# Performance work log

Measured on AMD Instinct MI355X. Metric: run time of the kernel, lower is better.

## Reference

```python
import jax, jax.numpy as jnp
import numpy as np

L = 12            # label_size (10 real tags + START + END)
START_ID = 10
END_ID = 11
V, E, T, B, HD = 32000, 512, 512, 64, 1024
H = HD // 2       # per-direction hidden size


def setup_inputs() -> dict:
    key = jax.random.key(0)
    ks = jax.random.split(key, 12)
    inp = {}
    inp['sents'] = jax.random.randint(ks[0], (B, T), 0, V)
    inp['labels'] = jax.random.randint(ks[1], (B, T), 0, L - 2)
    inp['lengths'] = jax.random.randint(ks[2], (B,), T // 2, T + 1)
    inp['embedding'] = jax.random.normal(ks[3], (V, E), jnp.float32) * 0.1
    s_ih = float(np.sqrt(6.0 / (4 * H + E)))
    s_hh = float(np.sqrt(6.0 / (4 * H + H)))
    # PyTorch LSTM gate order: i, f, g, o ; forget-gate bias init to 1 in each of
    # b_ih and b_hh -> combined bias has 2.0 in the forget slice.
    b = jnp.zeros((4 * H,), jnp.float32).at[H:2 * H].set(2.0)
    inp['w_ih_f'] = jax.random.uniform(ks[4], (4 * H, E), jnp.float32, -s_ih, s_ih)
    inp['w_hh_f'] = jax.random.uniform(ks[5], (4 * H, H), jnp.float32, -s_hh, s_hh)
    inp['b_f'] = b
    inp['w_ih_r'] = jax.random.uniform(ks[6], (4 * H, E), jnp.float32, -s_ih, s_ih)
    inp['w_hh_r'] = jax.random.uniform(ks[7], (4 * H, H), jnp.float32, -s_hh, s_hh)
    inp['b_r'] = b
    s_fc = float(np.sqrt(6.0 / (L + HD)))
    inp['fc_w'] = jax.random.uniform(ks[8], (L, HD), jnp.float32, -s_fc, s_fc)
    inp['fc_b'] = jnp.zeros((L,), jnp.float32)
    trans = jax.random.normal(ks[9], (L, L), jnp.float32)
    trans = trans.at[:, START_ID].set(-1000.0).at[END_ID, :].set(-1000.0)
    inp['transitions'] = trans
    return inp


def _lstm_dir(x, w_ih, w_hh, b, reverse):
    # x: [B, T, E] -> hidden states [B, T, H]; zero initial state.
    xg = jnp.einsum('bte,ge->btg', x, w_ih) + b  # [B, T, 4H] precomputed input gates
    if reverse:
        xg = xg[:, ::-1]
    h0 = jnp.zeros((x.shape[0], H), x.dtype)

    def step(carry, g):
        h, c = carry
        g = g + h @ w_hh.T
        i, f, gg, o = jnp.split(g, 4, axis=-1)
        c = jax.nn.sigmoid(f) * c + jax.nn.sigmoid(i) * jnp.tanh(gg)
        h = jax.nn.sigmoid(o) * jnp.tanh(c)
        return (h, c), h

    _, hs = jax.lax.scan(step, (h0, h0), jnp.swapaxes(xg, 0, 1))
    hs = jnp.swapaxes(hs, 0, 1)  # [B, T, H]
    if reverse:
        hs = hs[:, ::-1]
    return hs


def _features(sents, embedding, w_ih_f, w_hh_f, b_f, w_ih_r, w_hh_r, b_r, fc_w, fc_b):
    embeds = embedding[sents]  # [B, T, E]
    fwd = _lstm_dir(embeds, w_ih_f, w_hh_f, b_f, reverse=False)
    rev = _lstm_dir(embeds, w_ih_r, w_hh_r, b_r, reverse=True)
    out = jnp.tanh(jnp.concatenate([fwd, rev], axis=-1))  # [B, T, 2H]
    return jnp.einsum('bth,lh->btl', out, fc_w) + fc_b    # [B, T, L]


def _crf_log_z(feats, trans, lengths):
    # Batched forward algorithm; faithful to the original (alpha0 = zeros).
    def step(alpha, xs):
        feat_t, t = xs
        new = jax.nn.logsumexp(alpha[:, :, None] + trans[None] + feat_t[:, None, :], axis=1)
        return jnp.where((t < lengths)[:, None], new, alpha), None

    alpha0 = jnp.zeros((feats.shape[0], L), feats.dtype)
    alpha, _ = jax.lax.scan(step, alpha0, (jnp.swapaxes(feats, 0, 1), jnp.arange(feats.shape[1])))
    return jax.nn.logsumexp(alpha + trans[None, :, END_ID], axis=1)  # [B]


def _gold_scores(feats, trans, labels, lengths):
    Bv, Tv, _ = feats.shape
    lab_ext = jnp.concatenate([jnp.full((Bv, 1), START_ID, labels.dtype), labels], axis=1)
    prev, nxt = lab_ext[:, :-1], lab_ext[:, 1:]  # [B, T]
    emit = jnp.take_along_axis(feats, nxt[:, :, None], axis=2)[..., 0]
    tr = trans[prev, nxt]
    mask = (jnp.arange(Tv)[None, :] < lengths[:, None]).astype(feats.dtype)
    score = jnp.sum((emit + tr) * mask, axis=1)
    last = jnp.take_along_axis(labels, (lengths - 1)[:, None], axis=1)[:, 0]
    return score + trans[last, END_ID]  # [B]


def reference(sents, labels, lengths, embedding, w_ih_f, w_hh_f, b_f,
              w_ih_r, w_hh_r, b_r, fc_w, fc_b, transitions):
    feats = _features(sents, embedding, w_ih_f, w_hh_f, b_f, w_ih_r, w_hh_r, b_r, fc_w, fc_b)
    log_z = _crf_log_z(feats, transitions, lengths)
    gold = _gold_scores(feats, transitions, labels, lengths)
    return jnp.sum(log_z - gold)  # neg_log_likelihood summed over batch
```

## Files before the change

### kernel.cpp

```cpp
#include <hip/hip_runtime.h>
#include <stdint.h>

#define Bz 64
#define Tz 512
#define Ez 512
#define Hz 512
#define Lz 12
#define START_ID 10
#define END_ID 11

typedef unsigned int uint32;
typedef unsigned long long uint64;
typedef unsigned short ushort16;
typedef __bf16 bf16x8 __attribute__((ext_vector_type(8)));
typedef float f32x4 __attribute__((ext_vector_type(4)));

__device__ __forceinline__ float bf2f(uint32 u) {
    return __uint_as_float(u << 16);
}
__device__ __forceinline__ ushort16 f2bf(float f) {
    uint32 x = __float_as_uint(f);
    x += 0x7FFFu + ((x >> 16) & 1u);
    return (ushort16)(x >> 16);
}
__device__ __forceinline__ float sigf(float x) {
    return 1.0f / (1.0f + __expf(-x));
}
__device__ __forceinline__ float tanh_fast(float x) {
    return 1.0f - 2.0f / (__expf(2.0f * x) + 1.0f);
}
__device__ __forceinline__ bf16x8 packbf8(float4 a, float4 b) {
    union { ushort16 u[8]; bf16x8 v; } r;
    r.u[0] = f2bf(a.x); r.u[1] = f2bf(a.y); r.u[2] = f2bf(a.z); r.u[3] = f2bf(a.w);
    r.u[4] = f2bf(b.x); r.u[5] = f2bf(b.y); r.u[6] = f2bf(b.z); r.u[7] = f2bf(b.w);
    return r.v;
}

__global__ __launch_bounds__(256) void prepack_kernel(const int* __restrict__ sents,
                                                      const float* __restrict__ emb,
                                                      uint4* __restrict__ emb_p) {
    int c = blockIdx.x * 256 + threadIdx.x;
    int l   = c & 63;
    int kst = (c >> 6) & 15;
    int t   = (c >> 10) & 511;
    int bg  = c >> 19;
    int b   = (bg << 4) + (l & 15);
    int e0  = (kst << 5) + ((l >> 4) << 3);
    const float* p = emb + (size_t)sents[b * Tz + t] * Ez + e0;
    float4 f0 = *(const float4*)p;
    float4 f1 = *(const float4*)(p + 4);
    uint32 r0 = (uint32)f2bf(f0.x) | ((uint32)f2bf(f0.y) << 16);
    uint32 r1 = (uint32)f2bf(f0.z) | ((uint32)f2bf(f0.w) << 16);
    uint32 r2 = (uint32)f2bf(f1.x) | ((uint32)f2bf(f1.y) << 16);
    uint32 r3 = (uint32)f2bf(f1.z) | ((uint32)f2bf(f1.w) << 16);
    emb_p[c] = make_uint4(r0, r1, r2, r3);
}

__global__ __launch_bounds__(256, 1) void lstm_persist(
    const float* __restrict__ w_ih_f, const float* __restrict__ w_hh_f, const float* __restrict__ b_f,
    const float* __restrict__ w_ih_r, const float* __restrict__ w_hh_r, const float* __restrict__ b_r,
    const uint4* __restrict__ emb_p,
    ushort16* __restrict__ hs,
    uint32* __restrict__ h_pp,
    uint32* __restrict__ bar)
{
    const int bid = blockIdx.x;
    const int grp = bid & 7;
    const int d   = grp >> 2;
    const int bg  = grp & 3;
    const int ug  = bid >> 3;
    const int tid = threadIdx.x;
    const int w   = tid >> 6;
    const int l   = tid & 63;

    __shared__ __align__(16) char h_lds[16384];
    __shared__ float gx[2048];

    const float* Whh  = d ? w_hh_r : w_hh_f;
    const float* Wih  = d ? w_ih_r : w_ih_f;
    const float* bias = d ? b_r : b_f;
    const int u0 = ug << 5;

    bf16x8 Bih[2][16], Bhh[2][16];
    #pragma unroll
    for (int nn = 0; nn < 2; nn++) {
        const int wrow = (w << 9) + u0 + (nn << 4) + (l & 15);
        const int koff = (l >> 4) << 3;
        #pragma unroll
        for (int kst = 0; kst < 16; kst++) {
            const float* p = Wih + (size_t)wrow * Ez + (kst << 5) + koff;
            Bih[nn][kst] = packbf8(*(const float4*)p, *(const float4*)(p + 4));
            const float* q = Whh + (size_t)wrow * Hz + (kst << 5) + koff;
            Bhh[nn][kst] = packbf8(*(const float4*)q, *(const float4*)(q + 4));
        }
    }

    const int ab = tid >> 4;
    const int uw = tid & 15;
    const float bi0  = bias[u0 + 2*uw],        bi1  = bias[u0 + 2*uw + 1];
    const float bf0  = bias[512 + u0 + 2*uw],  bf1  = bias[512 + u0 + 2*uw + 1];
    const float bg0  = bias[1024 + u0 + 2*uw], bg1  = bias[1024 + u0 + 2*uw + 1];
    const float bo0  = bias[1536 + u0 + 2*uw], bo1  = bias[1536 + u0 + 2*uw + 1];
    float c0 = 0.0f, c1 = 0.0f;

    const int r16 = tid >> 4, seg = tid & 15;
    uint32* slot = bar + (((grp << 4) + ug) << 5);
    const uint64* h_pp64 = (const uint64*)h_pp;
    const uint4* xbase = emb_p + (((size_t)bg << 9) << 10);

    uint4 xf[16];
    {
        const uint4* xb = xbase + ((size_t)(d ? (Tz - 1) : 0) << 10) + l;
        #pragma unroll
        for (int kst = 0; kst < 16; kst++) xf[kst] = xb[(size_t)kst << 6];
    }

    for (int t = 0; t < Tz; t++) {
        const int tg = d ? (Tz - 1 - t) : t;

        f32x4 acc[2][2];
        #pragma unroll
        for (int nn = 0; nn < 2; nn++)
            #pragma unroll
            for (int i = 0; i < 2; i++) acc[nn][i] = (f32x4){0.f, 0.f, 0.f, 0.f};

        #pragma unroll
        for (int kst = 0; kst < 16; kst++) {
            union { uint4 q; bf16x8 v; } x;
            x.q = xf[kst];
            acc[0][kst & 1] = __builtin_amdgcn_mfma_f32_16x16x32_bf16(x.v, Bih[0][kst], acc[0][kst & 1], 0, 0, 0);
            acc[1][kst & 1] = __builtin_amdgcn_mfma_f32_16x16x32_bf16(x.v, Bih[1][kst], acc[1][kst & 1], 0, 0, 0);
        }

        if (t > 0) {
            if (tid < 64) {
                const uint32 tgt = (uint32)t;
                uint32* sl = bar + (((grp << 4) + (l & 15)) << 5);
                for (;;) {
                    uint32 v = tgt;
                    if (l < 16) v = __hip_atomic_load(sl, __ATOMIC_RELAXED, __HIP_MEMORY_SCOPE_AGENT);
                    if (__all((int)(v >= tgt))) break;
                    __builtin_amdgcn_s_sleep(1);
                }
            }
            __syncthreads();

            const uint64* hp = h_pp64 + ((size_t)((((t - 1) & 1) << 1) + d) * 64 + (bg << 4) + r16) * 128;
            #pragma unroll
            for (int jj = 0; jj < 8; jj++) {
                const int idx8 = (seg << 3) + jj;
                uint64 v = __hip_atomic_load(hp + idx8, __ATOMIC_RELAXED, __HIP_MEMORY_SCOPE_AGENT);
                *(uint64*)(h_lds + (r16 << 10) + ((((idx8 >> 1) << 4) ^ (r16 << 4))) + ((idx8 & 1) << 3)) = v;
            }
            __syncthreads();

            #pragma unroll
            for (int kst = 0; kst < 16; kst++) {
                bf16x8 a = *(const bf16x8*)(h_lds + ((l & 15) << 10) +
                            (((kst << 6) + ((l >> 4) << 4)) ^ ((l & 15) << 4)));
                acc[0][kst & 1] = __builtin_amdgcn_mfma_f32_16x16x32_bf16(a, Bhh[0][kst], acc[0][kst & 1], 0, 0, 0);
                acc[1][kst & 1] = __builtin_amdgcn_mfma_f32_16x16x32_bf16(a, Bhh[1][kst], acc[1][kst & 1], 0, 0, 0);
            }
        }

        f32x4 g0 = acc[0][0] + acc[0][1];
        f32x4 g1 = acc[1][0] + acc[1][1];

        #pragma unroll
        for (int r = 0; r < 4; r++) {
            const int b = ((l >> 4) << 2) + r;
            gx[(b << 7) + (w << 5) + (l & 15)] = g0[r];
            gx[(b << 7) + (w << 5) + 16 + (l & 15)] = g1[r];
        }
        __syncthreads();

        uint32 hval;
        {
            const int base = (ab << 7) + (uw << 1);
            float gi_0 = gx[base],      gi_1 = gx[base + 1];
            float gf_0 = gx[base + 32], gf_1 = gx[base + 33];
            float gg_0 = gx[base + 64], gg_1 = gx[base + 65];
            float go_0 = gx[base + 96], go_1 = gx[base + 97];
            c0 = sigf(gf_0 + bf0) * c0 + sigf(gi_0 + bi0) * tanh_fast(gg_0 + bg0);
            float hn0 = sigf(go_0 + bo0) * tanh_fast(c0);
            c1 = sigf(gf_1 + bf1) * c1 + sigf(gi_1 + bi1) * tanh_fast(gg_1 + bg1);
            float hn1 = sigf(go_1 + bo1) * tanh_fast(c1);
            hval = (uint32)f2bf(hn0) | ((uint32)f2bf(hn1) << 16);
            const size_t pidx = ((size_t)(((t & 1) << 1) + d) * 64 + (bg << 4) + ab) * 256 + (ug << 4) + uw;
            __hip_atomic_store(h_pp + pidx, hval, __ATOMIC_RELAXED, __HIP_MEMORY_SCOPE_AGENT);
        }
        asm volatile("s_waitcnt vmcnt(0)" ::: "memory");
        __syncthreads();
        if (tid == 0)
            __hip_atomic_store(slot, (uint32)(t + 1), __ATOMIC_RELAXED, __HIP_MEMORY_SCOPE_AGENT);

        {
            const size_t hrow = (((size_t)(d << 6) + (bg << 4) + ab) * 512 + tg) * 512 + u0 + (uw << 1);
            *(uint32*)(hs + hrow) = hval;
        }
        if (t < Tz - 1) {
            const int tg2 = d ? (Tz - 2 - t) : (t + 1);
            const uint4* xb = xbase + ((size_t)tg2 << 10) + l;
            #pragma unroll
            for (int kst = 0; kst < 16; kst++) xf[kst] = xb[(size_t)kst << 6];
        }
    }
}

__global__ __launch_bounds__(256) void feat_kernel(const ushort16* __restrict__ hs,
                                                   const float* __restrict__ fc_w,
                                                   const float* __restrict__ fc_b,
                                                   float* __restrict__ feats) {
    const int m = blockIdx.x * 4 + (threadIdx.x >> 6);
    const int lane = threadIdx.x & 63;

    const ushort16* hf = hs + (size_t)m * Hz + lane * 8;
    const ushort16* hr = hs + (size_t)Bz * Tz * Hz + (size_t)m * Hz + lane * 8;
    uint4 vf = *(const uint4*)hf;
    uint4 vr = *(const uint4*)hr;

    float x[16];
    {
        uint32 w0 = vf.x, w1 = vf.y, w2 = vf.z, w3 = vf.w;
        x[0] = tanh_fast(bf2f(w0 & 0xFFFFu)); x[1] = tanh_fast(bf2f(w0 >> 16));
        x[2] = tanh_fast(bf2f(w1 & 0xFFFFu)); x[3] = tanh_fast(bf2f(w1 >> 16));
        x[4] = tanh_fast(bf2f(w2 & 0xFFFFu)); x[5] = tanh_fast(bf2f(w2 >> 16));
        x[6] = tanh_fast(bf2f(w3 & 0xFFFFu)); x[7] = tanh_fast(bf2f(w3 >> 16));
        w0 = vr.x; w1 = vr.y; w2 = vr.z; w3 = vr.w;
        x[8]  = tanh_fast(bf2f(w0 & 0xFFFFu)); x[9]  = tanh_fast(bf2f(w0 >> 16));
        x[10] = tanh_fast(bf2f(w1 & 0xFFFFu)); x[11] = tanh_fast(bf2f(w1 >> 16));
        x[12] = tanh_fast(bf2f(w2 & 0xFFFFu)); x[13] = tanh_fast(bf2f(w2 >> 16));
        x[14] = tanh_fast(bf2f(w3 & 0xFFFFu)); x[15] = tanh_fast(bf2f(w3 >> 16));
    }

    float out = 0.0f;
    #pragma unroll
    for (int ll = 0; ll < Lz; ll++) {
        const float* wf = fc_w + (size_t)ll * 1024 + lane * 8;
        const float* wr = wf + 512;
        float4 a0 = *(const float4*)wf;
        float4 a1 = *(const float4*)(wf + 4);
        float4 b0 = *(const float4*)wr;
        float4 b1 = *(const float4*)(wr + 4);
        float s = a0.x * x[0] + a0.y * x[1] + a0.z * x[2] + a0.w * x[3]
                + a1.x * x[4] + a1.y * x[5] + a1.z * x[6] + a1.w * x[7]
                + b0.x * x[8] + b0.y * x[9] + b0.z * x[10] + b0.w * x[11]
                + b1.x * x[12] + b1.y * x[13] + b1.z * x[14] + b1.w * x[15];
        #pragma unroll
        for (int off = 32; off; off >>= 1) s += __shfl_xor(s, off);
        if (lane == ll) out = s + fc_b[ll];
    }
    if (lane < Lz) feats[(size_t)m * Lz + lane] = out;
}

__global__ __launch_bounds__(64) void crf_kernel(const float* __restrict__ feats,
                                                 const float* __restrict__ trans,
                                                 const int* __restrict__ labels,
                                                 const int* __restrict__ lengths,
                                                 float* __restrict__ res) {
    const int b = blockIdx.x;
    const int lane = threadIdx.x;
    const int jj = (lane < Lz) ? lane : 0;

    float tcol[12];
    #pragma unroll
    for (int i = 0; i < 12; i++) tcol[i] = trans[i * Lz + jj];
    const int len = lengths[b];

    float alpha = 0.0f;
    for (int t = 0; t < Tz; t++) {
        float feat = feats[((size_t)b * Tz + t) * Lz + jj];
        float v[12];
        #pragma unroll
        for (int i = 0; i < 12; i++) v[i] = __shfl(alpha, i) + tcol[i];
        float m = v[0];
        #pragma unroll
        for (int i = 1; i < 12; i++) m = fmaxf(m, v[i]);
        float s = 0.0f;
        #pragma unroll
        for (int i = 0; i < 12; i++) s += __expf(v[i] - m);
        float newa = feat + m + __logf(s);
        if (t < len && lane < Lz) alpha = newa;
    }

    float val = (lane < Lz) ? (alpha + trans[jj * Lz + END_ID]) : -INFINITY;
    float m = val;
    #pragma unroll
    for (int off = 32; off; off >>= 1) m = fmaxf(m, __shfl_xor(m, off));
    float s = (lane < Lz) ? __expf(val - m) : 0.0f;
    #pragma unroll
    for (int off = 32; off; off >>= 1) s += __shfl_xor(s, off);
    float log_z = m + __logf(s);

    float g = 0.0f;
    for (int t = lane; t < Tz; t += 64) {
        if (t < len) {
            int nxt = labels[b * Tz + t];
            int prev = (t == 0) ? START_ID : labels[b * Tz + t - 1];
            g += feats[((size_t)b * Tz + t) * Lz + nxt] + trans[prev * Lz + nxt];
        }
    }
    #pragma unroll
    for (int off = 32; off; off >>= 1) g += __shfl_xor(g, off);
    int last = labels[b * Tz + len - 1];
    float gold = g + trans[last * Lz + END_ID];

    if (lane == 0) res[b] = log_z - gold;
}

__global__ __launch_bounds__(64) void reduce_kernel(const float* __restrict__ res,
                                                    float* __restrict__ out) {
    float v = res[threadIdx.x];
    #pragma unroll
    for (int off = 32; off; off >>= 1) v += __shfl_xor(v, off);
    if (threadIdx.x == 0) out[0] = v;
}

extern "C" void kernel_launch(void* const* d_in, const int* in_sizes, int n_in,
                              void* d_out, int out_size, void* d_ws, size_t ws_size,
                              hipStream_t stream) {
    const int*   sents     = (const int*)d_in[0];
    const int*   labels    = (const int*)d_in[1];
    const int*   lengths   = (const int*)d_in[2];
    const float* embedding = (const float*)d_in[3];
    const float* w_ih_f    = (const float*)d_in[4];
    const float* w_hh_f    = (const float*)d_in[5];
    const float* b_f       = (const float*)d_in[6];
    const float* w_ih_r    = (const float*)d_in[7];
    const float* w_hh_r    = (const float*)d_in[8];
    const float* b_r       = (const float*)d_in[9];
    const float* fc_w      = (const float*)d_in[10];
    const float* fc_b      = (const float*)d_in[11];
    const float* trans     = (const float*)d_in[12];
    (void)in_sizes; (void)n_in; (void)out_size; (void)ws_size;

    char* ws = (char*)d_ws;
    size_t off = 0;
    uint4*    emb_p = (uint4*)(ws + off);    off += (size_t)4 * 512 * 16 * 64 * 16;
    ushort16* hs    = (ushort16*)(ws + off); off += (size_t)2 * Bz * Tz * Hz * 2;
    float*    feats = (float*)(ws + off);    off += (size_t)Bz * Tz * Lz * 4;
    uint32*   h_pp  = (uint32*)(ws + off);   off += (size_t)2 * 2 * Bz * 256 * 4;
    uint32*   bar   = (uint32*)(ws + off);   off += 16384;
    float*    res   = (float*)(ws + off);    off += Bz * 4;

    hipMemsetAsync(bar, 0, 16384, stream);
    prepack_kernel<<<8192, 256, 0, stream>>>(sents, embedding, emb_p);
    lstm_persist<<<128, 256, 0, stream>>>(w_ih_f, w_hh_f, b_f, w_ih_r, w_hh_r, b_r,
                                          emb_p, hs, h_pp, bar);
    feat_kernel<<<8192, 256, 0, stream>>>(hs, fc_w, fc_b, feats);
    crf_kernel<<<64, 64, 0, stream>>>(feats, trans, labels, lengths, res);
    reduce_kernel<<<1, 64, 0, stream>>>(res, (float*)d_out);
}
```

Before: 2.171 ms.

## Fold batch groups into each LSTM block, shrinking persistent grid to 32 blocks

```diff
diff --git a/kernel.cpp b/kernel.cpp
--- a/kernel.cpp
+++ b/kernel.cpp
@@ -65,14 +65,13 @@
     uint32* __restrict__ bar)
 {
     const int bid = blockIdx.x;
-    const int grp = bid & 7;
-    const int d   = grp >> 2;
-    const int bg  = grp & 3;
-    const int ug  = bid >> 3;
+    const int d   = bid >> 4;
+    const int ug  = bid & 15;
     const int tid = threadIdx.x;
     const int w   = tid >> 6;
     const int l   = tid & 63;
 
+    __shared__ __align__(16) char x_lds[4][16384];
     __shared__ __align__(16) char h_lds[16384];
     __shared__ float gx[2048];
 
@@ -101,108 +100,116 @@
     const float bf0  = bias[512 + u0 + 2*uw],  bf1  = bias[512 + u0 + 2*uw + 1];
     const float bg0  = bias[1024 + u0 + 2*uw], bg1  = bias[1024 + u0 + 2*uw + 1];
     const float bo0  = bias[1536 + u0 + 2*uw], bo1  = bias[1536 + u0 + 2*uw + 1];
-    float c0 = 0.0f, c1 = 0.0f;
+    float cc0[4] = {0.f, 0.f, 0.f, 0.f};
+    float cc1[4] = {0.f, 0.f, 0.f, 0.f};
 
     const int r16 = tid >> 4, seg = tid & 15;
-    uint32* slot = bar + (((grp << 4) + ug) << 5);
+    uint32* slot = bar + (((d << 4) + ug) << 5);
     const uint64* h_pp64 = (const uint64*)h_pp;
-    const uint4* xbase = emb_p + (((size_t)bg << 9) << 10);
-
-    uint4 xf[16];
-    {
-        const uint4* xb = xbase + ((size_t)(d ? (Tz - 1) : 0) << 10) + l;
-        #pragma unroll
-        for (int kst = 0; kst < 16; kst++) xf[kst] = xb[(size_t)kst << 6];
-    }
 
     for (int t = 0; t < Tz; t++) {
         const int tg = d ? (Tz - 1 - t) : t;
 
-        f32x4 acc[2][2];
-        #pragma unroll
-        for (int nn = 0; nn < 2; nn++)
+        {
+            const int kst = (w << 2);
             #pragma unroll
-            for (int i = 0; i < 2; i++) acc[nn][i] = (f32x4){0.f, 0.f, 0.f, 0.f};
-
-        #pragma unroll
-        for (int kst = 0; kst < 16; kst++) {
-            union { uint4 q; bf16x8 v; } x;
-            x.q = xf[kst];
-            acc[0][kst & 1] = __builtin_amdgcn_mfma_f32_16x16x32_bf16(x.v, Bih[0][kst], acc[0][kst & 1], 0, 0, 0);
-            acc[1][kst & 1] = __builtin_amdgcn_mfma_f32_16x16x32_bf16(x.v, Bih[1][kst], acc[1][kst & 1], 0, 0, 0);
+            for (int bg = 0; bg < 4; bg++) {
+                #pragma unroll
+                for (int j = 0; j < 4; j++) {
+                    const int k = kst + j;
+                    const uint4* src = emb_p + ((size_t)bg << 19) + ((size_t)tg << 10) + (k << 6) + l;
+                    char* dst = &x_lds[bg][k << 10];
+                    __builtin_amdgcn_global_load_lds(
+                        (const __attribute__((address_space(1))) void*)src,
+                        (__attribute__((address_space(3))) void*)dst, 16, 0, 0);
+                }
+            }
+            asm volatile("s_waitcnt vmcnt(0)" ::: "memory");
+            __syncthreads();
         }
 
-        if (t > 0) {
-            if (tid < 64) {
-                const uint32 tgt = (uint32)t;
-                uint32* sl = bar + (((grp << 4) + (l & 15)) << 5);
-                for (;;) {
-                    uint32 v = tgt;
-                    if (l < 16) v = __hip_atomic_load(sl, __ATOMIC_RELAXED, __HIP_MEMORY_SCOPE_AGENT);
-                    if (__all((int)(v >= tgt))) break;
-                    __builtin_amdgcn_s_sleep(1);
-                }
-            }
-            __syncthreads();
-
-            const uint64* hp = h_pp64 + ((size_t)((((t - 1) & 1) << 1) + d) * 64 + (bg << 4) + r16) * 128;
+        #pragma unroll
+        for (int bg = 0; bg < 4; bg++) {
+            f32x4 acc0[2], acc1[2];
             #pragma unroll
-            for (int jj = 0; jj < 8; jj++) {
-                const int idx8 = (seg << 3) + jj;
-                uint64 v = __hip_atomic_load(hp + idx8, __ATOMIC_RELAXED, __HIP_MEMORY_SCOPE_AGENT);
-                *(uint64*)(h_lds + (r16 << 10) + ((((idx8 >> 1) << 4) ^ (r16 << 4))) + ((idx8 & 1) << 3)) = v;
-            }
-            __syncthreads();
+            for (int i = 0; i < 2; i++) {
+                acc0[i] = (f32x4){0.f, 0.f, 0.f, 0.f};
+                acc1[i] = (f32x4){0.f, 0.f, 0.f, 0.f};
+            }
 
             #pragma unroll
             for (int kst = 0; kst < 16; kst++) {
-                bf16x8 a = *(const bf16x8*)(h_lds + ((l & 15) << 10) +
-                            (((kst << 6) + ((l >> 4) << 4)) ^ ((l & 15) << 4)));
-                acc[0][kst & 1] = __builtin_amdgcn_mfma_f32_16x16x32_bf16(a, Bhh[0][kst], acc[0][kst & 1], 0, 0, 0);
-                acc[1][kst & 1] = __builtin_amdgcn_mfma_f32_16x16x32_bf16(a, Bhh[1][kst], acc[1][kst & 1], 0, 0, 0);
-            }
-        }
-
-        f32x4 g0 = acc[0][0] + acc[0][1];
-        f32x4 g1 = acc[1][0] + acc[1][1];
-
-        #pragma unroll
-        for (int r = 0; r < 4; r++) {
-            const int b = ((l >> 4) << 2) + r;
-            gx[(b << 7) + (w << 5) + (l & 15)] = g0[r];
-            gx[(b << 7) + (w << 5) + 16 + (l & 15)] = g1[r];
-        }
-        __syncthreads();
-
-        uint32 hval;
-        {
-            const int base = (ab << 7) + (uw << 1);
-            float gi_0 = gx[base],      gi_1 = gx[base + 1];
-            float gf_0 = gx[base + 32], gf_1 = gx[base + 33];
-            float gg_0 = gx[base + 64], gg_1 = gx[base + 65];
-            float go_0 = gx[base + 96], go_1 = gx[base + 97];
-            c0 = sigf(gf_0 + bf0) * c0 + sigf(gi_0 + bi0) * tanh_fast(gg_0 + bg0);
-            float hn0 = sigf(go_0 + bo0) * tanh_fast(c0);
-            c1 = sigf(gf_1 + bf1) * c1 + sigf(gi_1 + bi1) * tanh_fast(gg_1 + bg1);
-            float hn1 = sigf(go_1 + bo1) * tanh_fast(c1);
-            hval = (uint32)f2bf(hn0) | ((uint32)f2bf(hn1) << 16);
-            const size_t pidx = ((size_t)(((t & 1) << 1) + d) * 64 + (bg << 4) + ab) * 256 + (ug << 4) + uw;
-            __hip_atomic_store(h_pp + pidx, hval, __ATOMIC_RELAXED, __HIP_MEMORY_SCOPE_AGENT);
-        }
-        asm volatile("s_waitcnt vmcnt(0)" ::: "memory");
-        __syncthreads();
-        if (tid == 0)
-            __hip_atomic_store(slot, (uint32)(t + 1), __ATOMIC_RELAXED, __HIP_MEMORY_SCOPE_AGENT);
-
-        {
-            const size_t hrow = (((size_t)(d << 6) + (bg << 4) + ab) * 512 + tg) * 512 + u0 + (uw << 1);
-            *(uint32*)(hs + hrow) = hval;
-        }
-        if (t < Tz - 1) {
-            const int tg2 = d ? (Tz - 2 - t) : (t + 1);
-            const uint4* xb = xbase + ((size_t)tg2 << 10) + l;
+                bf16x8 xa = *(const bf16x8*)(&x_lds[bg][(kst << 10) + (l << 4)]);
+                acc0[kst & 1] = __builtin_amdgcn_mfma_f32_16x16x32_bf16(xa, Bih[0][kst], acc0[kst & 1], 0, 0, 0);
+                acc1[kst & 1] = __builtin_amdgcn_mfma_f32_16x16x32_bf16(xa, Bih[1][kst], acc1[kst & 1], 0, 0, 0);
+            }
+
+            if (t > 0) {
+                if (tid < 64) {
+                    const uint32 tgt = (uint32)(4 * (t - 1) + bg + 1);
+                    uint32* sl = bar + (((d << 4) + (l & 15)) << 5);
+                    for (;;) {
+                        uint32 v = tgt;
+                        if (l < 16) v = __hip_atomic_load(sl, __ATOMIC_RELAXED, __HIP_MEMORY_SCOPE_AGENT);
+                        if (__all((int)(v >= tgt))) break;
+                        __builtin_amdgcn_s_sleep(1);
+                    }
+                }
+                __syncthreads();
+
+                const uint64* hp = h_pp64 + ((size_t)((((t - 1) & 1) << 1) + d) * 64 + (bg << 4) + r16) * 128;
+                #pragma unroll
+                for (int jj = 0; jj < 8; jj++) {
+                    const int idx8 = (seg << 3) + jj;
+                    uint64 v = __hip_atomic_load(hp + idx8, __ATOMIC_RELAXED, __HIP_MEMORY_SCOPE_AGENT);
+                    *(uint64*)(h_lds + (r16 << 10) + ((((idx8 >> 1) << 4) ^ (r16 << 4))) + ((idx8 & 1) << 3)) = v;
+                }
+                __syncthreads();
+
+                #pragma unroll
+                for (int kst = 0; kst < 16; kst++) {
+                    bf16x8 a = *(const bf16x8*)(h_lds + ((l & 15) << 10) +
+                                (((kst << 6) + ((l >> 4) << 4)) ^ ((l & 15) << 4)));
+                    acc0[kst & 1] = __builtin_amdgcn_mfma_f32_16x16x32_bf16(a, Bhh[0][kst], acc0[kst & 1], 0, 0, 0);
+                    acc1[kst & 1] = __builtin_amdgcn_mfma_f32_16x16x32_bf16(a, Bhh[1][kst], acc1[kst & 1], 0, 0, 0);
+                }
+            }
+
+            f32x4 g0 = acc0[0] + acc0[1];
+            f32x4 g1 = acc1[0] + acc1[1];
+
             #pragma unroll
-            for (int kst = 0; kst < 16; kst++) xf[kst] = xb[(size_t)kst << 6];
+            for (int r = 0; r < 4; r++) {
+                const int b = ((l >> 4) << 2) + r;
+                gx[(b << 7) + (w << 5) + (l & 15)] = g0[r];
+                gx[(b << 7) + (w << 5) + 16 + (l & 15)] = g1[r];
+            }
+            __syncthreads();
+
+            uint32 hval;
+            {
+                const int base = (ab << 7) + (uw << 1);
+                float gi_0 = gx[base],      gi_1 = gx[base + 1];
+                float gf_0 = gx[base + 32], gf_1 = gx[base + 33];
+                float gg_0 = gx[base + 64], gg_1 = gx[base + 65];
+                float go_0 = gx[base + 96], go_1 = gx[base + 97];
+                cc0[bg] = sigf(gf_0 + bf0) * cc0[bg] + sigf(gi_0 + bi0) * tanh_fast(gg_0 + bg0);
+                float hn0 = sigf(go_0 + bo0) * tanh_fast(cc0[bg]);
+                cc1[bg] = sigf(gf_1 + bf1) * cc1[bg] + sigf(gi_1 + bi1) * tanh_fast(gg_1 + bg1);
+                float hn1 = sigf(go_1 + bo1) * tanh_fast(cc1[bg]);
+                hval = (uint32)f2bf(hn0) | ((uint32)f2bf(hn1) << 16);
+                const size_t pidx = ((size_t)(((t & 1) << 1) + d) * 64 + (bg << 4) + ab) * 256 + (ug << 4) + uw;
+                __hip_atomic_store(h_pp + pidx, hval, __ATOMIC_RELAXED, __HIP_MEMORY_SCOPE_AGENT);
+            }
+            asm volatile("s_waitcnt vmcnt(0)" ::: "memory");
+            __syncthreads();
+            if (tid == 0)
+                __hip_atomic_store(slot, (uint32)(4 * t + bg + 1), __ATOMIC_RELAXED, __HIP_MEMORY_SCOPE_AGENT);
+
+            {
+                const size_t hrow = (((size_t)(d << 6) + (bg << 4) + ab) * 512 + tg) * 512 + u0 + (uw << 1);
+                *(uint32*)(hs + hrow) = hval;
+            }
         }
     }
 }
@@ -345,8 +352,8 @@
 
     hipMemsetAsync(bar, 0, 16384, stream);
     prepack_kernel<<<8192, 256, 0, stream>>>(sents, embedding, emb_p);
-    lstm_persist<<<128, 256, 0, stream>>>(w_ih_f, w_hh_f, b_f, w_ih_r, w_hh_r, b_r,
-                                          emb_p, hs, h_pp, bar);
+    lstm_persist<<<32, 256, 0, stream>>>(w_ih_f, w_hh_f, b_f, w_ih_r, w_hh_r, b_r,
+                                         emb_p, hs, h_pp, bar);
     feat_kernel<<<8192, 256, 0, stream>>>(hs, fc_w, fc_b, feats);
     crf_kernel<<<64, 64, 0, stream>>>(feats, trans, labels, lengths, res);
     reduce_kernel<<<1, 64, 0, stream>>>(res, (float*)d_out);
```

New measurement: 8.506 ms. 292% more time.

## Replace flag barrier with step-tagged hidden-state publication polled directly

Applied to the files above, without the earlier changes.

```diff
diff --git a/kernel.cpp b/kernel.cpp
--- a/kernel.cpp
+++ b/kernel.cpp
@@ -61,8 +61,7 @@
     const float* __restrict__ w_ih_r, const float* __restrict__ w_hh_r, const float* __restrict__ b_r,
     const uint4* __restrict__ emb_p,
     ushort16* __restrict__ hs,
-    uint32* __restrict__ h_pp,
-    uint32* __restrict__ bar)
+    uint64* __restrict__ h_ppT)
 {
     const int bid = blockIdx.x;
     const int grp = bid & 7;
@@ -75,6 +74,7 @@
 
     __shared__ __align__(16) char h_lds[16384];
     __shared__ float gx[2048];
+    __shared__ uint32 h_stage[256];
 
     const float* Whh  = d ? w_hh_r : w_hh_f;
     const float* Wih  = d ? w_ih_r : w_ih_f;
@@ -104,8 +104,6 @@
     float c0 = 0.0f, c1 = 0.0f;
 
     const int r16 = tid >> 4, seg = tid & 15;
-    uint32* slot = bar + (((grp << 4) + ug) << 5);
-    const uint64* h_pp64 = (const uint64*)h_pp;
     const uint4* xbase = emb_p + (((size_t)bg << 9) << 10);
 
     uint4 xf[16];
@@ -118,39 +116,57 @@
     for (int t = 0; t < Tz; t++) {
         const int tg = d ? (Tz - 1 - t) : t;
 
-        f32x4 acc[2][2];
-        #pragma unroll
-        for (int nn = 0; nn < 2; nn++)
+        uint64 hv[16];
+        uint64* hp = h_ppT + ((size_t)((((t - 1) & 1) << 1) + d) * 64 + (bg << 4) + r16) * 256 + (seg << 4);
+        if (t > 0 && seg != ug) {
             #pragma unroll
-            for (int i = 0; i < 2; i++) acc[nn][i] = (f32x4){0.f, 0.f, 0.f, 0.f};
+            for (int i = 0; i < 16; i++)
+                hv[i] = __hip_atomic_load(hp + i, __ATOMIC_RELAXED, __HIP_MEMORY_SCOPE_AGENT);
+        }
+
+        f32x4 acc0[2], acc1[2];
+        #pragma unroll
+        for (int i = 0; i < 2; i++) {
+            acc0[i] = (f32x4){0.f, 0.f, 0.f, 0.f};
+            acc1[i] = (f32x4){0.f, 0.f, 0.f, 0.f};
+        }
 
         #pragma unroll
         for (int kst = 0; kst < 16; kst++) {
             union { uint4 q; bf16x8 v; } x;
             x.q = xf[kst];
-            acc[0][kst & 1] = __builtin_amdgcn_mfma_f32_16x16x32_bf16(x.v, Bih[0][kst], acc[0][kst & 1], 0, 0, 0);
-            acc[1][kst & 1] = __builtin_amdgcn_mfma_f32_16x16x32_bf16(x.v, Bih[1][kst], acc[1][kst & 1], 0, 0, 0);
+            acc0[kst & 1] = __builtin_amdgcn_mfma_f32_16x16x32_bf16(x.v, Bih[0][kst], acc0[kst & 1], 0, 0, 0);
+            acc1[kst & 1] = __builtin_amdgcn_mfma_f32_16x16x32_bf16(x.v, Bih[1][kst], acc1[kst & 1], 0, 0, 0);
         }
 
         if (t > 0) {
-            if (tid < 64) {
-                const uint32 tgt = (uint32)t;
-                uint32* sl = bar + (((grp << 4) + (l & 15)) << 5);
+            const uint32 want = (uint32)(t - 1);
+            uint32 hd[16];
+            if (seg != ug) {
+                int guard = 0;
                 for (;;) {
-                    uint32 v = tgt;
-                    if (l < 16) v = __hip_atomic_load(sl, __ATOMIC_RELAXED, __HIP_MEMORY_SCOPE_AGENT);
-                    if (__all((int)(v >= tgt))) break;
-                    __builtin_amdgcn_s_sleep(1);
+                    bool bad = false;
+                    #pragma unroll
+                    for (int i = 0; i < 16; i++) {
+                        if ((uint32)(hv[i] >> 32) != want) {
+                            hv[i] = __hip_atomic_load(hp + i, __ATOMIC_RELAXED, __HIP_MEMORY_SCOPE_AGENT);
+                            bad = true;
+                        }
+                    }
+                    if (!bad || ++guard > 4096) break;
                 }
+                #pragma unroll
+                for (int i = 0; i < 16; i++) hd[i] = (uint32)hv[i];
+            } else {
+                #pragma unroll
+                for (int i = 0; i < 16; i++) hd[i] = h_stage[(r16 << 4) + i];
             }
-            __syncthreads();
-
-            const uint64* hp = h_pp64 + ((size_t)((((t - 1) & 1) << 1) + d) * 64 + (bg << 4) + r16) * 128;
+
             #pragma unroll
-            for (int jj = 0; jj < 8; jj++) {
-                const int idx8 = (seg << 3) + jj;
-                uint64 v = __hip_atomic_load(hp + idx8, __ATOMIC_RELAXED, __HIP_MEMORY_SCOPE_AGENT);
-                *(uint64*)(h_lds + (r16 << 10) + ((((idx8 >> 1) << 4) ^ (r16 << 4))) + ((idx8 & 1) << 3)) = v;
+            for (int i = 0; i < 16; i++) {
+                const int dj = (seg << 4) + i;
+                const int cj = dj >> 2;
+                *(uint32*)(h_lds + (r16 << 10) + (((cj << 4) ^ (r16 << 4))) + ((dj & 3) << 2)) = hd[i];
             }
             __syncthreads();
 
@@ -158,13 +174,13 @@
             for (int kst = 0; kst < 16; kst++) {
                 bf16x8 a = *(const bf16x8*)(h_lds + ((l & 15) << 10) +
                             (((kst << 6) + ((l >> 4) << 4)) ^ ((l & 15) << 4)));
-                acc[0][kst & 1] = __builtin_amdgcn_mfma_f32_16x16x32_bf16(a, Bhh[0][kst], acc[0][kst & 1], 0, 0, 0);
-                acc[1][kst & 1] = __builtin_amdgcn_mfma_f32_16x16x32_bf16(a, Bhh[1][kst], acc[1][kst & 1], 0, 0, 0);
+                acc0[kst & 1] = __builtin_amdgcn_mfma_f32_16x16x32_bf16(a, Bhh[0][kst], acc0[kst & 1], 0, 0, 0);
+                acc1[kst & 1] = __builtin_amdgcn_mfma_f32_16x16x32_bf16(a, Bhh[1][kst], acc1[kst & 1], 0, 0, 0);
             }
         }
 
-        f32x4 g0 = acc[0][0] + acc[0][1];
-        f32x4 g1 = acc[1][0] + acc[1][1];
+        f32x4 g0 = acc0[0] + acc0[1];
+        f32x4 g1 = acc1[0] + acc1[1];
 
         #pragma unroll
         for (int r = 0; r < 4; r++) {
@@ -187,12 +203,10 @@
             float hn1 = sigf(go_1 + bo1) * tanh_fast(c1);
             hval = (uint32)f2bf(hn0) | ((uint32)f2bf(hn1) << 16);
             const size_t pidx = ((size_t)(((t & 1) << 1) + d) * 64 + (bg << 4) + ab) * 256 + (ug << 4) + uw;
-            __hip_atomic_store(h_pp + pidx, hval, __ATOMIC_RELAXED, __HIP_MEMORY_SCOPE_AGENT);
-        }
-        asm volatile("s_waitcnt vmcnt(0)" ::: "memory");
-        __syncthreads();
-        if (tid == 0)
-            __hip_atomic_store(slot, (uint32)(t + 1), __ATOMIC_RELAXED, __HIP_MEMORY_SCOPE_AGENT);
+            uint64 pub = ((uint64)(uint32)t << 32) | (uint64)hval;
+            __hip_atomic_store(h_ppT + pidx, pub, __ATOMIC_RELAXED, __HIP_MEMORY_SCOPE_AGENT);
+            h_stage[(ab << 4) + uw] = hval;
+        }
 
         {
             const size_t hrow = (((size_t)(d << 6) + (bg << 4) + ab) * 512 + tg) * 512 + u0 + (uw << 1);
@@ -204,6 +218,7 @@
             #pragma unroll
             for (int kst = 0; kst < 16; kst++) xf[kst] = xb[(size_t)kst << 6];
         }
+        __syncthreads();
     }
 }
 
@@ -339,14 +354,12 @@
     uint4*    emb_p = (uint4*)(ws + off);    off += (size_t)4 * 512 * 16 * 64 * 16;
     ushort16* hs    = (ushort16*)(ws + off); off += (size_t)2 * Bz * Tz * Hz * 2;
     float*    feats = (float*)(ws + off);    off += (size_t)Bz * Tz * Lz * 4;
-    uint32*   h_pp  = (uint32*)(ws + off);   off += (size_t)2 * 2 * Bz * 256 * 4;
-    uint32*   bar   = (uint32*)(ws + off);   off += 16384;
+    uint64*   h_ppT = (uint64*)(ws + off);   off += (size_t)2 * 2 * Bz * 256 * 8;
     float*    res   = (float*)(ws + off);    off += Bz * 4;
 
-    hipMemsetAsync(bar, 0, 16384, stream);
     prepack_kernel<<<8192, 256, 0, stream>>>(sents, embedding, emb_p);
     lstm_persist<<<128, 256, 0, stream>>>(w_ih_f, w_hh_f, b_f, w_ih_r, w_hh_r, b_r,
-                                          emb_p, hs, h_pp, bar);
+                                          emb_p, hs, h_ppT);
     feat_kernel<<<8192, 256, 0, stream>>>(hs, fc_w, fc_b, feats);
     crf_kernel<<<64, 64, 0, stream>>>(feats, trans, labels, lengths, res);
     reduce_kernel<<<1, 64, 0, stream>>>(res, (float*)d_out);
```

After: 2.723 ms. 25.4% more time.

## Tighten cross-block spin wait, reuse local h slice, defer input MFMAs

Applied to the files above, without the earlier changes.

```diff
diff --git a/kernel.cpp b/kernel.cpp
--- a/kernel.cpp
+++ b/kernel.cpp
@@ -75,6 +75,7 @@
 
     __shared__ __align__(16) char h_lds[16384];
     __shared__ float gx[2048];
+    __shared__ uint32 h_stage[256];
 
     const float* Whh  = d ? w_hh_r : w_hh_f;
     const float* Wih  = d ? w_ih_r : w_ih_f;
@@ -118,39 +119,43 @@
     for (int t = 0; t < Tz; t++) {
         const int tg = d ? (Tz - 1 - t) : t;
 
-        f32x4 acc[2][2];
-        #pragma unroll
-        for (int nn = 0; nn < 2; nn++)
-            #pragma unroll
-            for (int i = 0; i < 2; i++) acc[nn][i] = (f32x4){0.f, 0.f, 0.f, 0.f};
-
-        #pragma unroll
-        for (int kst = 0; kst < 16; kst++) {
-            union { uint4 q; bf16x8 v; } x;
-            x.q = xf[kst];
-            acc[0][kst & 1] = __builtin_amdgcn_mfma_f32_16x16x32_bf16(x.v, Bih[0][kst], acc[0][kst & 1], 0, 0, 0);
-            acc[1][kst & 1] = __builtin_amdgcn_mfma_f32_16x16x32_bf16(x.v, Bih[1][kst], acc[1][kst & 1], 0, 0, 0);
+        f32x4 acc0[2], acc1[2];
+        #pragma unroll
+        for (int i = 0; i < 2; i++) {
+            acc0[i] = (f32x4){0.f, 0.f, 0.f, 0.f};
+            acc1[i] = (f32x4){0.f, 0.f, 0.f, 0.f};
         }
 
         if (t > 0) {
             if (tid < 64) {
                 const uint32 tgt = (uint32)t;
                 uint32* sl = bar + (((grp << 4) + (l & 15)) << 5);
+                int guard = 0;
                 for (;;) {
                     uint32 v = tgt;
                     if (l < 16) v = __hip_atomic_load(sl, __ATOMIC_RELAXED, __HIP_MEMORY_SCOPE_AGENT);
                     if (__all((int)(v >= tgt))) break;
-                    __builtin_amdgcn_s_sleep(1);
+                    if (++guard > (1 << 14)) break;
                 }
             }
             __syncthreads();
 
+            uint64 hv8[8];
             const uint64* hp = h_pp64 + ((size_t)((((t - 1) & 1) << 1) + d) * 64 + (bg << 4) + r16) * 128;
+            if (seg != ug) {
+                #pragma unroll
+                for (int jj = 0; jj < 8; jj++)
+                    hv8[jj] = __hip_atomic_load(hp + (seg << 3) + jj, __ATOMIC_RELAXED, __HIP_MEMORY_SCOPE_AGENT);
+            } else {
+                #pragma unroll
+                for (int jj = 0; jj < 8; jj++)
+                    hv8[jj] = (uint64)h_stage[(r16 << 4) + (jj << 1)]
+                            | ((uint64)h_stage[(r16 << 4) + (jj << 1) + 1] << 32);
+            }
             #pragma unroll
             for (int jj = 0; jj < 8; jj++) {
                 const int idx8 = (seg << 3) + jj;
-                uint64 v = __hip_atomic_load(hp + idx8, __ATOMIC_RELAXED, __HIP_MEMORY_SCOPE_AGENT);
-                *(uint64*)(h_lds + (r16 << 10) + ((((idx8 >> 1) << 4) ^ (r16 << 4))) + ((idx8 & 1) << 3)) = v;
+                *(uint64*)(h_lds + (r16 << 10) + ((((idx8 >> 1) << 4) ^ (r16 << 4))) + ((idx8 & 1) << 3)) = hv8[jj];
             }
             __syncthreads();
 
@@ -158,13 +163,21 @@
             for (int kst = 0; kst < 16; kst++) {
                 bf16x8 a = *(const bf16x8*)(h_lds + ((l & 15) << 10) +
                             (((kst << 6) + ((l >> 4) << 4)) ^ ((l & 15) << 4)));
-                acc[0][kst & 1] = __builtin_amdgcn_mfma_f32_16x16x32_bf16(a, Bhh[0][kst], acc[0][kst & 1], 0, 0, 0);
-                acc[1][kst & 1] = __builtin_amdgcn_mfma_f32_16x16x32_bf16(a, Bhh[1][kst], acc[1][kst & 1], 0, 0, 0);
+                acc0[kst & 1] = __builtin_amdgcn_mfma_f32_16x16x32_bf16(a, Bhh[0][kst], acc0[kst & 1], 0, 0, 0);
+                acc1[kst & 1] = __builtin_amdgcn_mfma_f32_16x16x32_bf16(a, Bhh[1][kst], acc1[kst & 1], 0, 0, 0);
             }
         }
 
-        f32x4 g0 = acc[0][0] + acc[0][1];
-        f32x4 g1 = acc[1][0] + acc[1][1];
+        #pragma unroll
+        for (int kst = 0; kst < 16; kst++) {
+            union { uint4 q; bf16x8 v; } x;
+            x.q = xf[kst];
+            acc0[kst & 1] = __builtin_amdgcn_mfma_f32_16x16x32_bf16(x.v, Bih[0][kst], acc0[kst & 1], 0, 0, 0);
+            acc1[kst & 1] = __builtin_amdgcn_mfma_f32_16x16x32_bf16(x.v, Bih[1][kst], acc1[kst & 1], 0, 0, 0);
+        }
+
+        f32x4 g0 = acc0[0] + acc0[1];
+        f32x4 g1 = acc1[0] + acc1[1];
 
         #pragma unroll
         for (int r = 0; r < 4; r++) {
@@ -186,6 +199,7 @@
             c1 = sigf(gf_1 + bf1) * c1 + sigf(gi_1 + bi1) * tanh_fast(gg_1 + bg1);
             float hn1 = sigf(go_1 + bo1) * tanh_fast(c1);
             hval = (uint32)f2bf(hn0) | ((uint32)f2bf(hn1) << 16);
+            h_stage[(ab << 4) + uw] = hval;
             const size_t pidx = ((size_t)(((t & 1) << 1) + d) * 64 + (bg << 4) + ab) * 256 + (ug << 4) + uw;
             __hip_atomic_store(h_pp + pidx, hval, __ATOMIC_RELAXED, __HIP_MEMORY_SCOPE_AGENT);
         }
```

Result: faster. 2.060 ms (median of 2 runs) (-5.1%).
